# Kernel tuning notes

Hardware: AMD Instinct MI355X
Metric: run time of the kernel (lower is better)

The kernel has to match this reference:

```python
import jax, jax.numpy as jnp
import numpy as np
import math

NUM_BUCKETS = 32
MAX_DISTANCE = 128


def _relative_position_bucket(relative_position):
    # Unidirectional (bidirectional=False): rp = max(-relative_position, 0)
    rp = jnp.maximum(-relative_position, 0)
    max_exact = NUM_BUCKETS // 2  # 16
    is_small = rp < max_exact
    rp_f = jnp.maximum(rp, 1).astype(jnp.float32)
    large = max_exact + (
        jnp.log(rp_f / max_exact) / math.log(MAX_DISTANCE / max_exact)
        * (NUM_BUCKETS - max_exact)
    ).astype(jnp.int32)
    large = jnp.minimum(large, NUM_BUCKETS - 1)
    return jnp.where(is_small, rp, large)


def _t5_rel_bias(bias_table, T):
    # bias_table: [num_buckets, n_heads] -> [1, n_heads, T, T]
    ctx = jnp.arange(T, dtype=jnp.int32)[:, None]
    mem = jnp.arange(T, dtype=jnp.int32)[None, :]
    buckets = _relative_position_bucket(mem - ctx)  # [T, T]
    values = bias_table[buckets]  # [T, T, H]
    return jnp.transpose(values, (2, 0, 1))[None]  # [1, H, T, T]


def setup_inputs() -> dict:
    key = jax.random.key(0)
    ks = jax.random.split(key, 6)
    B, T, C, H = 2, 2048, 1024, 16
    x = jax.random.normal(ks[0], (B, T, C), dtype=jnp.float32)
    W_attn = jax.random.normal(ks[1], (C, 3 * C), dtype=jnp.float32) * 0.02
    b_attn = jnp.zeros((3 * C,), dtype=jnp.float32)
    W_proj = jax.random.normal(ks[2], (C, C), dtype=jnp.float32) * 0.02
    b_proj = jnp.zeros((C,), dtype=jnp.float32)
    bias_table = jax.random.normal(ks[3], (NUM_BUCKETS, H), dtype=jnp.float32) * 0.02
    return {"x": x, "W_attn": W_attn, "b_attn": b_attn,
            "W_proj": W_proj, "b_proj": b_proj, "bias_table": bias_table}


def reference(x, W_attn, b_attn, W_proj, b_proj, bias_table):
    B, T, C = x.shape
    H = bias_table.shape[1]
    D = C // H
    qkv = x @ W_attn + b_attn  # [B, T, 3C]
    q, k, v = jnp.split(qkv, 3, axis=-1)
    # [B, T, C] -> [B, H, T, D]
    q = q.reshape(B, T, H, D).transpose(0, 2, 1, 3)
    k = k.reshape(B, T, H, D).transpose(0, 2, 1, 3)
    v = v.reshape(B, T, H, D).transpose(0, 2, 1, 3)
    rel_bias = _t5_rel_bias(bias_table, T)  # [1, H, T, T]
    att = jnp.einsum('bhtd,bhsd->bhts', q, k) * (1.0 / math.sqrt(D))
    att = att + rel_bias
    causal = jnp.tril(jnp.ones((T, T), dtype=bool))
    att = jnp.where(causal, att, -jnp.inf)
    att = jax.nn.softmax(att, axis=-1)
    y = jnp.einsum('bhts,bhsd->bhtd', att, v)  # [B, H, T, D]
    y = y.transpose(0, 2, 1, 3).reshape(B, T, C)
    return y @ W_proj + b_proj
```

## Files before the change

kernel.cpp:

```cpp
#include <hip/hip_runtime.h>
#include <hip/hip_bf16.h>
#include <math.h>

typedef __attribute__((ext_vector_type(4))) float f32x4;
typedef __attribute__((ext_vector_type(8))) __bf16 bf16x8;
typedef __attribute__((ext_vector_type(4))) __bf16 bf16x4;

#define DEVI __device__ __forceinline__

DEVI f32x4 mfma16(bf16x8 a, bf16x8 b, f32x4 c) {
  return __builtin_amdgcn_mfma_f32_16x16x32_bf16(a, b, c, 0, 0, 0);
}

DEVI void gload16(const void* g, void* l) {
  __builtin_amdgcn_global_load_lds(
      (const __attribute__((address_space(1))) void*)g,
      (__attribute__((address_space(3))) void*)l, 16, 0, 0);
}

DEVI float exp2a(float x) {
  float r;
  asm("v_exp_f32 %0, %1" : "=v"(r) : "v"(x));
  return r;
}

#define LOG2E 1.4426950408889634f
#define QSCALE 0.18033688011110793f
#define FIXMAX 8.0f

__global__ __launch_bounds__(256) void prep_k(
    const float* __restrict__ x, const float* __restrict__ W_attn,
    const float* __restrict__ W_proj, const float* __restrict__ bt,
    __bf16* __restrict__ xb, __bf16* __restrict__ WaT,
    __bf16* __restrict__ WpT, float* __restrict__ tbl) {
  __shared__ float tile[32][33];
  int bid = blockIdx.x;
  const int t = threadIdx.x;
  if (bid < 4096) {
    int i = (bid * 256 + t) * 4;
    float4 v = *(const float4*)&x[i];
    bf16x4 o = {(__bf16)v.x, (__bf16)v.y, (__bf16)v.z, (__bf16)v.w};
    *(bf16x4*)&xb[i] = o;
    return;
  }
  bid -= 4096;
  if (bid < 4096) {
    const float* in;
    __bf16* out;
    int Cc, bx, by;
    if (bid < 3072) {
      in = W_attn; out = WaT; Cc = 3072; bx = bid % 96; by = bid / 96;
    } else {
      int b2 = bid - 3072;
      in = W_proj; out = WpT; Cc = 1024; bx = b2 % 32; by = b2 / 32;
    }
    const int R = 1024;
    int tx = t & 31, ty = t >> 5;
    int xcol = bx * 32 + tx;
    for (int r = ty; r < 32; r += 8)
      tile[r][tx] = in[(size_t)(by * 32 + r) * Cc + xcol];
    __syncthreads();
    int xo = by * 32 + tx;
    for (int r = ty; r < 32; r += 8)
      out[(size_t)(bx * 32 + r) * R + xo] = (__bf16)tile[tx][r];
    return;
  }
  bid -= 4096;
  int idx = bid * 256 + t;
  int h = idx >> 11, rp = idx & 2047;
  int bucket;
  if (rp < 16) {
    bucket = rp;
  } else {
    float v = (logf((float)rp * 0.0625f) / 2.0794415416798357f) * 16.0f;
    bucket = 16 + (int)v;
    if (bucket > 31) bucket = 31;
  }
  tbl[idx] = bt[bucket * 16 + h] * LOG2E;
}

template <int MODE>
__global__ __launch_bounds__(256) void gemm_bf16(
    const __bf16* __restrict__ A, const __bf16* __restrict__ BT,
    const float* __restrict__ bias, float* __restrict__ outF,
    __bf16* __restrict__ qb, __bf16* __restrict__ kb, __bf16* __restrict__ vtb,
    int M, int N, int K) {
  __shared__ __align__(16) __bf16 lA[2][128 * 32];
  __shared__ __align__(16) __bf16 lB[2][128 * 32];
  const int t = threadIdx.x;
  const int w = t >> 6, lane = t & 63;
  const int m0 = blockIdx.x * 128, n0 = blockIdx.y * 128;
  const int wr = (w >> 1) * 64, wc = (w & 1) * 64;

  f32x4 acc[4][4] = {};

  const int rA = lane & 15;
  const int kk = (lane >> 4) * 8;

  auto STAGE = [&](int buf, int k0) {
#pragma unroll
    for (int r = 0; r < 2; ++r) {
      int c = r * 256 + t;
      int row = c >> 2, cc = c & 3;
      gload16(A + (size_t)(m0 + row) * K + k0 + cc * 8,
              &lA[buf][(r * 256 + w * 64) * 8]);
      gload16(BT + (size_t)(n0 + row) * K + k0 + cc * 8,
              &lB[buf][(r * 256 + w * 64) * 8]);
    }
  };

  STAGE(0, 0);
  int cur = 0;
  for (int k0 = 0; k0 < K; k0 += 32, cur ^= 1) {
    __syncthreads();
    if (k0 + 32 < K) STAGE(cur ^ 1, k0 + 32);
    bf16x8 af[4], bfr[4];
#pragma unroll
    for (int i = 0; i < 4; ++i)
      af[i] = *(const bf16x8*)&lA[cur][(wr + i * 16 + rA) * 32 + kk];
#pragma unroll
    for (int j = 0; j < 4; ++j)
      bfr[j] = *(const bf16x8*)&lB[cur][(wc + j * 16 + rA) * 32 + kk];
#pragma unroll
    for (int i = 0; i < 4; ++i)
#pragma unroll
      for (int j = 0; j < 4; ++j)
        acc[i][j] = mfma16(af[i], bfr[j], acc[i][j]);
  }

  const int colb = n0 + wc + rA;
  const int rowb = m0 + wr + (lane >> 4) * 4;
#pragma unroll
  for (int j = 0; j < 4; ++j) {
    int n = colb + j * 16;
    float bv = bias[n];
#pragma unroll
    for (int i = 0; i < 4; ++i) {
#pragma unroll
      for (int e = 0; e < 4; ++e) {
        int m = rowb + i * 16 + e;
        float v = acc[i][j][e] + bv;
        if constexpr (MODE == 0) {
          int b = m >> 11, tt = m & 2047;
          int sec = n >> 10, nn = n & 1023;
          int h = nn >> 6, d = nn & 63;
          if (sec == 0)
            qb[(((size_t)(b * 16 + h)) * 2048 + tt) * 64 + d] = (__bf16)(v * QSCALE);
          else if (sec == 1)
            kb[(((size_t)(b * 16 + h)) * 2048 + tt) * 64 + d] = (__bf16)v;
          else
            vtb[(((size_t)(b * 16 + h)) * 64 + d) * 2048 + tt] = (__bf16)v;
        } else {
          outF[(size_t)m * N + n] = v;
        }
      }
    }
  }
}

__global__ __launch_bounds__(256) void attn_k(
    const __bf16* __restrict__ q, const __bf16* __restrict__ k,
    const __bf16* __restrict__ vt, const float* __restrict__ tbl,
    __bf16* __restrict__ y) {
  __shared__ __align__(16) __bf16 lK[2][64 * 64];
  __shared__ __align__(16) __bf16 lV[2][64 * 64];
  __shared__ __align__(16) __bf16 lPT[4][16 * 64];
  __shared__ float lb[2][128];

  const int t = threadIdx.x, w = t >> 6, lane = t & 63;
  const int bh = blockIdx.x, b = bh >> 4, h = bh & 15;
  const int p = blockIdx.y;
  const int kq = lane >> 4, ncol = lane & 15;
  const int sw = (ncol & 7);

  const __bf16* qp = q + (size_t)bh * 2048 * 64;
  const __bf16* kp = k + (size_t)bh * 2048 * 64;
  const __bf16* vp = vt + (size_t)bh * 64 * 2048;
  const float* tb = tbl + h * 2048;
  const float bconst = tb[2047] - FIXMAX;

  __bf16* Pw = &lPT[w][0];

  auto STAGE = [&](int buf, int qt_, int jt_) {
#pragma unroll
    for (int r = 0; r < 2; ++r) {
      int c = r * 256 + t;
      int row = c >> 3, cc = c & 7;
      int sc = cc ^ (row & 7);
      gload16(kp + (size_t)(jt_ * 64 + row) * 64 + sc * 8,
              &lK[buf][(r * 256 + w * 64) * 8]);
      gload16(vp + (size_t)row * 2048 + jt_ * 64 + sc * 8,
              &lV[buf][(r * 256 + w * 64) * 8]);
    }
    int dt_ = qt_ - jt_;
    if (dt_ < 3 && t < 128) {
      int rb = dt_ * 64 - 63 + t;
      lb[buf][t] = tb[rb < 0 ? 0 : rb] - FIXMAX;
    }
  };

  const int qts[2] = {31 - p, p};
  int cur = 0;
  STAGE(0, qts[0], 0);

  for (int seg = 0; seg < 2; ++seg) {
    const int qt = qts[seg];
    const int qbase = qt * 64 + w * 16;
    bf16x8 qf0 = *(const bf16x8*)&qp[(size_t)(qbase + ncol) * 64 + kq * 8];
    bf16x8 qf1 = *(const bf16x8*)&qp[(size_t)(qbase + ncol) * 64 + kq * 8 + 32];

    f32x4 O[4] = {};
    float lsum = 0.f;

    for (int jt = 0; jt <= qt; ++jt, cur ^= 1) {
      const int dt = qt - jt;
      const int rel = 4 * dt + w;
      __syncthreads();
      if (jt < qt) STAGE(cur ^ 1, qt, jt + 1);
      else if (seg == 0) STAGE(cur ^ 1, qts[1], 0);

      const __bf16* Kc = lK[cur];
      const float* lbc = lb[cur];
      const bool useb = (dt >= 3);

      const int idxb = 63 + w * 16 + ncol - 4 * kq;
#pragma unroll
      for (int fn = 0; fn < 4; ++fn) {
        bf16x4 pb;
        if (fn <= rel) {
          f32x4 s;
          if (useb) {
            s = (f32x4){bconst, bconst, bconst, bconst};
          } else {
#pragma unroll
            for (int i = 0; i < 4; ++i) s[i] = lbc[idxb - fn * 16 - i];
            if (fn == rel) {
#pragma unroll
              for (int i = 0; i < 4; ++i)
                if (ncol - 4 * kq - i < 0) s[i] = -1e30f;
            }
          }
          int row = fn * 16 + ncol;
          bf16x8 kf0 = *(const bf16x8*)((const char*)Kc + row * 128 + ((kq ^ sw) * 16));
          bf16x8 kf1 = *(const bf16x8*)((const char*)Kc + row * 128 + (((4 + kq) ^ sw) * 16));
          s = mfma16(kf0, qf0, s);
          s = mfma16(kf1, qf1, s);
#pragma unroll
          for (int i = 0; i < 4; ++i) {
            float pe = exp2a(s[i]);
            lsum += pe;
            pb[i] = (__bf16)pe;
          }
        } else {
          pb = (bf16x4){(__bf16)0.f, (__bf16)0.f, (__bf16)0.f, (__bf16)0.f};
        }
        *(bf16x4*)((char*)Pw + ncol * 128 + ((32 * fn + 8 * kq) ^ (sw << 4))) = pb;
      }
      asm volatile("s_waitcnt lgkmcnt(0)" ::: "memory");
      __builtin_amdgcn_sched_barrier(0);

      const __bf16* Vc = lV[cur];
      const int kf2max = (rel >= 2) ? 2 : 1;
      for (int kf2 = 0; kf2 < kf2max; ++kf2) {
        bf16x8 pf = *(const bf16x8*)((const char*)Pw + ncol * 128 +
                                     (((4 * kf2 + kq) ^ sw) * 16));
#pragma unroll
        for (int fd = 0; fd < 4; ++fd) {
          int vrow = fd * 16 + ncol;
          bf16x8 vf = *(const bf16x8*)((const char*)Vc + vrow * 128 +
                                       (((4 * kf2 + kq) ^ sw) * 16));
          O[fd] = mfma16(pf, vf, O[fd]);
        }
      }
    }

    float ls = lsum;
    ls += __shfl_xor(ls, 16);
    ls += __shfl_xor(ls, 32);
#pragma unroll
    for (int i = 0; i < 4; ++i) {
      float li = __shfl(ls, 4 * kq + i);
      float rinv = 1.0f / li;
      int row = qbase + 4 * kq + i;
#pragma unroll
      for (int fd = 0; fd < 4; ++fd) {
        int col = h * 64 + fd * 16 + ncol;
        y[((size_t)(b * 2048 + row)) * 1024 + col] = (__bf16)(O[fd][i] * rinv);
      }
    }
  }
}


extern "C" void kernel_launch(void* const* d_in, const int* in_sizes, int n_in,
                              void* d_out, int out_size, void* d_ws, size_t ws_size,
                              hipStream_t stream) {
  const float* x = (const float*)d_in[0];
  const float* W_attn = (const float*)d_in[1];
  const float* b_attn = (const float*)d_in[2];
  const float* W_proj = (const float*)d_in[3];
  const float* b_proj = (const float*)d_in[4];
  const float* bias_table = (const float*)d_in[5];
  float* out = (float*)d_out;

  char* ws = (char*)d_ws;
  __bf16* xb   = (__bf16*)(ws + 0);
  __bf16* WaT  = (__bf16*)(ws + 8388608);
  __bf16* WpT  = (__bf16*)(ws + 14680064);
  __bf16* qb   = (__bf16*)(ws + 16777216);
  __bf16* kb   = (__bf16*)(ws + 25165824);
  __bf16* vtb  = (__bf16*)(ws + 33554432);
  __bf16* yb   = (__bf16*)(ws + 41943040);
  float*  tbl  = (float*)(ws + 50331648);

  prep_k<<<8320, 256, 0, stream>>>(x, W_attn, W_proj, bias_table,
                                   xb, WaT, WpT, tbl);
  gemm_bf16<0><<<dim3(32, 24), 256, 0, stream>>>(xb, WaT, b_attn, nullptr,
                                                 qb, kb, vtb, 4096, 3072, 1024);
  attn_k<<<dim3(32, 16), 256, 0, stream>>>(qb, kb, vtb, tbl, yb);
  gemm_bf16<1><<<dim3(32, 8), 256, 0, stream>>>(yb, WpT, b_proj, out,
                                                nullptr, nullptr, nullptr,
                                                4096, 1024, 1024);
}
```

Measured before the change: 124.5 us.

## Launch one attention block per query tile and drop K/V double buffering

Each attention block now handles a single 64-row query tile, so the grid doubles and the earlier pairing of tiles qt and 31-qt for load balance goes away. The K/V/bias LDS staging drops from double buffering to a single buffer, loaded synchronously with a barrier before compute. Blocks use about half the LDS and should fit more per CU, but global loads no longer overlap with compute, and block lengths become uneven, which the hardware scheduler has to balance.

Result: faster. 119.0 us (-4.4%).

```diff
diff --git a/kernel.cpp b/kernel.cpp
--- a/kernel.cpp
+++ b/kernel.cpp
@@ -162,14 +162,15 @@
     const __bf16* __restrict__ q, const __bf16* __restrict__ k,
     const __bf16* __restrict__ vt, const float* __restrict__ tbl,
     __bf16* __restrict__ y) {
-  __shared__ __align__(16) __bf16 lK[2][64 * 64];
-  __shared__ __align__(16) __bf16 lV[2][64 * 64];
+  __shared__ __align__(16) __bf16 lK[64 * 64];
+  __shared__ __align__(16) __bf16 lV[64 * 64];
   __shared__ __align__(16) __bf16 lPT[4][16 * 64];
-  __shared__ float lb[2][128];
+  __shared__ float lb[128];
 
   const int t = threadIdx.x, w = t >> 6, lane = t & 63;
   const int bh = blockIdx.x, b = bh >> 4, h = bh & 15;
-  const int p = blockIdx.y;
+  const int qt = 31 - blockIdx.y;
+  const int qbase = qt * 64 + w * 16;
   const int kq = lane >> 4, ncol = lane & 15;
   const int sw = (ncol & 7);
 
@@ -181,112 +182,95 @@
 
   __bf16* Pw = &lPT[w][0];
 
-  auto STAGE = [&](int buf, int qt_, int jt_) {
+  bf16x8 qf0 = *(const bf16x8*)&qp[(size_t)(qbase + ncol) * 64 + kq * 8];
+  bf16x8 qf1 = *(const bf16x8*)&qp[(size_t)(qbase + ncol) * 64 + kq * 8 + 32];
+
+  f32x4 O[4] = {};
+  float lsum = 0.f;
+
+  for (int jt = 0; jt <= qt; ++jt) {
+    const int dt = qt - jt;
+    const int rel = 4 * dt + w;
+    __syncthreads();
 #pragma unroll
     for (int r = 0; r < 2; ++r) {
       int c = r * 256 + t;
       int row = c >> 3, cc = c & 7;
       int sc = cc ^ (row & 7);
-      gload16(kp + (size_t)(jt_ * 64 + row) * 64 + sc * 8,
-              &lK[buf][(r * 256 + w * 64) * 8]);
-      gload16(vp + (size_t)row * 2048 + jt_ * 64 + sc * 8,
-              &lV[buf][(r * 256 + w * 64) * 8]);
-    }
-    int dt_ = qt_ - jt_;
-    if (dt_ < 3 && t < 128) {
-      int rb = dt_ * 64 - 63 + t;
-      lb[buf][t] = tb[rb < 0 ? 0 : rb] - FIXMAX;
-    }
-  };
-
-  const int qts[2] = {31 - p, p};
-  int cur = 0;
-  STAGE(0, qts[0], 0);
-
-  for (int seg = 0; seg < 2; ++seg) {
-    const int qt = qts[seg];
-    const int qbase = qt * 64 + w * 16;
-    bf16x8 qf0 = *(const bf16x8*)&qp[(size_t)(qbase + ncol) * 64 + kq * 8];
-    bf16x8 qf1 = *(const bf16x8*)&qp[(size_t)(qbase + ncol) * 64 + kq * 8 + 32];
-
-    f32x4 O[4] = {};
-    float lsum = 0.f;
-
-    for (int jt = 0; jt <= qt; ++jt, cur ^= 1) {
-      const int dt = qt - jt;
-      const int rel = 4 * dt + w;
-      __syncthreads();
-      if (jt < qt) STAGE(cur ^ 1, qt, jt + 1);
-      else if (seg == 0) STAGE(cur ^ 1, qts[1], 0);
-
-      const __bf16* Kc = lK[cur];
-      const float* lbc = lb[cur];
-      const bool useb = (dt >= 3);
-
-      const int idxb = 63 + w * 16 + ncol - 4 * kq;
-#pragma unroll
-      for (int fn = 0; fn < 4; ++fn) {
-        bf16x4 pb;
-        if (fn <= rel) {
-          f32x4 s;
-          if (useb) {
-            s = (f32x4){bconst, bconst, bconst, bconst};
-          } else {
-#pragma unroll
-            for (int i = 0; i < 4; ++i) s[i] = lbc[idxb - fn * 16 - i];
-            if (fn == rel) {
-#pragma unroll
-              for (int i = 0; i < 4; ++i)
-                if (ncol - 4 * kq - i < 0) s[i] = -1e30f;
-            }
+      gload16(kp + (size_t)(jt * 64 + row) * 64 + sc * 8,
+              &lK[(r * 256 + w * 64) * 8]);
+      gload16(vp + (size_t)row * 2048 + jt * 64 + sc * 8,
+              &lV[(r * 256 + w * 64) * 8]);
+    }
+    if (dt < 3 && t < 128) {
+      int rb = dt * 64 - 63 + t;
+      lb[t] = tb[rb < 0 ? 0 : rb] - FIXMAX;
+    }
+    __syncthreads();
+
+    const bool useb = (dt >= 3);
+
+    const int idxb = 63 + w * 16 + ncol - 4 * kq;
+#pragma unroll
+    for (int fn = 0; fn < 4; ++fn) {
+      bf16x4 pb;
+      if (fn <= rel) {
+        f32x4 s;
+        if (useb) {
+          s = (f32x4){bconst, bconst, bconst, bconst};
+        } else {
+#pragma unroll
+          for (int i = 0; i < 4; ++i) s[i] = lb[idxb - fn * 16 - i];
+          if (fn == rel) {
+#pragma unroll
+            for (int i = 0; i < 4; ++i)
+              if (ncol - 4 * kq - i < 0) s[i] = -1e30f;
           }
-          int row = fn * 16 + ncol;
-          bf16x8 kf0 = *(const bf16x8*)((const char*)Kc + row * 128 + ((kq ^ sw) * 16));
-          bf16x8 kf1 = *(const bf16x8*)((const char*)Kc + row * 128 + (((4 + kq) ^ sw) * 16));
-          s = mfma16(kf0, qf0, s);
-          s = mfma16(kf1, qf1, s);
-#pragma unroll
-          for (int i = 0; i < 4; ++i) {
-            float pe = exp2a(s[i]);
-            lsum += pe;
-            pb[i] = (__bf16)pe;
-          }
-        } else {
-          pb = (bf16x4){(__bf16)0.f, (__bf16)0.f, (__bf16)0.f, (__bf16)0.f};
         }
-        *(bf16x4*)((char*)Pw + ncol * 128 + ((32 * fn + 8 * kq) ^ (sw << 4))) = pb;
+        int row = fn * 16 + ncol;
+        bf16x8 kf0 = *(const bf16x8*)((const char*)lK + row * 128 + ((kq ^ sw) * 16));
+        bf16x8 kf1 = *(const bf16x8*)((const char*)lK + row * 128 + (((4 + kq) ^ sw) * 16));
+        s = mfma16(kf0, qf0, s);
+        s = mfma16(kf1, qf1, s);
+#pragma unroll
+        for (int i = 0; i < 4; ++i) {
+          float pe = exp2a(s[i]);
+          lsum += pe;
+          pb[i] = (__bf16)pe;
+        }
+      } else {
+        pb = (bf16x4){(__bf16)0.f, (__bf16)0.f, (__bf16)0.f, (__bf16)0.f};
       }
-      asm volatile("s_waitcnt lgkmcnt(0)" ::: "memory");
-      __builtin_amdgcn_sched_barrier(0);
-
-      const __bf16* Vc = lV[cur];
-      const int kf2max = (rel >= 2) ? 2 : 1;
-      for (int kf2 = 0; kf2 < kf2max; ++kf2) {
-        bf16x8 pf = *(const bf16x8*)((const char*)Pw + ncol * 128 +
+      *(bf16x4*)((char*)Pw + ncol * 128 + ((32 * fn + 8 * kq) ^ (sw << 4))) = pb;
+    }
+    asm volatile("s_waitcnt lgkmcnt(0)" ::: "memory");
+    __builtin_amdgcn_sched_barrier(0);
+
+    const int kf2max = (rel >= 2) ? 2 : 1;
+    for (int kf2 = 0; kf2 < kf2max; ++kf2) {
+      bf16x8 pf = *(const bf16x8*)((const char*)Pw + ncol * 128 +
+                                   (((4 * kf2 + kq) ^ sw) * 16));
+#pragma unroll
+      for (int fd = 0; fd < 4; ++fd) {
+        int vrow = fd * 16 + ncol;
+        bf16x8 vf = *(const bf16x8*)((const char*)lV + vrow * 128 +
                                      (((4 * kf2 + kq) ^ sw) * 16));
-#pragma unroll
-        for (int fd = 0; fd < 4; ++fd) {
-          int vrow = fd * 16 + ncol;
-          bf16x8 vf = *(const bf16x8*)((const char*)Vc + vrow * 128 +
-                                       (((4 * kf2 + kq) ^ sw) * 16));
-          O[fd] = mfma16(pf, vf, O[fd]);
-        }
+        O[fd] = mfma16(pf, vf, O[fd]);
       }
     }
-
-    float ls = lsum;
-    ls += __shfl_xor(ls, 16);
-    ls += __shfl_xor(ls, 32);
-#pragma unroll
-    for (int i = 0; i < 4; ++i) {
-      float li = __shfl(ls, 4 * kq + i);
-      float rinv = 1.0f / li;
-      int row = qbase + 4 * kq + i;
-#pragma unroll
-      for (int fd = 0; fd < 4; ++fd) {
-        int col = h * 64 + fd * 16 + ncol;
-        y[((size_t)(b * 2048 + row)) * 1024 + col] = (__bf16)(O[fd][i] * rinv);
-      }
+  }
+
+  lsum += __shfl_xor(lsum, 16);
+  lsum += __shfl_xor(lsum, 32);
+#pragma unroll
+  for (int i = 0; i < 4; ++i) {
+    float li = __shfl(lsum, 4 * kq + i);
+    float rinv = 1.0f / li;
+    int row = qbase + 4 * kq + i;
+#pragma unroll
+    for (int fd = 0; fd < 4; ++fd) {
+      int col = h * 64 + fd * 16 + ncol;
+      y[((size_t)(b * 2048 + row)) * 1024 + col] = (__bf16)(O[fd][i] * rinv);
     }
   }
 }
@@ -317,7 +301,7 @@
                                    xb, WaT, WpT, tbl);
   gemm_bf16<0><<<dim3(32, 24), 256, 0, stream>>>(xb, WaT, b_attn, nullptr,
                                                  qb, kb, vtb, 4096, 3072, 1024);
-  attn_k<<<dim3(32, 16), 256, 0, stream>>>(qb, kb, vtb, tbl, yb);
+  attn_k<<<dim3(32, 32), 256, 0, stream>>>(qb, kb, vtb, tbl, yb);
   gemm_bf16<1><<<dim3(32, 8), 256, 0, stream>>>(yb, WpT, b_proj, out,
                                                 nullptr, nullptr, nullptr,
                                                 4096, 1024, 1024);
```
